# Kernel tuning notes

Measured on AMD Instinct MI355X. Metric: run time of the kernel, lower is better.

## Reference

```python
import jax, jax.numpy as jnp
import numpy as np

N, E, D, C, M = 50000, 600000, 128, 40, 25000


def setup_inputs() -> dict:
    key = jax.random.key(0)
    ks = jax.random.split(key, 10)
    s = 1.0 / np.sqrt(D)
    return {
        "x": jax.random.normal(ks[0], (N, D), jnp.float32),
        "edge_index": jax.random.randint(ks[1], (2, E), 0, N, jnp.int64),
        "node_label_index": jax.random.randint(ks[2], (M,), 0, N, jnp.int64),
        "W0": jax.random.normal(ks[3], (D, D), jnp.float32) * s,
        "b0": jnp.zeros((D,), jnp.float32),
        "W1": jax.random.normal(ks[4], (D, D), jnp.float32) * s,
        "b1": jnp.zeros((D,), jnp.float32),
        "W2": jax.random.normal(ks[5], (D, D), jnp.float32) * s,
        "b2": jnp.zeros((D,), jnp.float32),
        "W3": jax.random.normal(ks[6], (D, D), jnp.float32) * s,
        "b3": jnp.zeros((D,), jnp.float32),
        "Wh": jax.random.normal(ks[7], (D, C), jnp.float32) * s,
        "bh": jnp.zeros((C,), jnp.float32),
    }


def _gcn(x, W, b, src, dst, dinv):
    h = x @ W                                    # [N, D']
    norm = (dinv[src] * dinv[dst])[:, None]      # [E, 1]
    agg = jax.ops.segment_sum(h[src] * norm, dst, num_segments=x.shape[0])
    return agg + h * (dinv ** 2)[:, None] + b    # self-loop term + bias


def reference(x, edge_index, node_label_index, W0, b0, W1, b1, W2, b2, W3, b3, Wh, bh):
    src, dst = edge_index[0], edge_index[1]
    # degree with self-loops (PyG counts in-degree on dst after add_self_loops)
    deg = 1.0 + jax.ops.segment_sum(jnp.ones((src.shape[0],), x.dtype), dst,
                                    num_segments=x.shape[0])
    dinv = jax.lax.rsqrt(deg)

    cell0 = _gcn(x, W0, b0, src, dst, dinv)
    cell1 = _gcn(jax.nn.relu(cell0), W1, b1, src, dst, dinv)
    cell2 = (_gcn(jax.nn.relu(cell0), W2, b2, src, dst, dinv)
             + _gcn(jax.nn.relu(cell1), W2, b2, src, dst, dinv))
    cell3 = (_gcn(jax.nn.relu(cell0), W3, b3, src, dst, dinv)
             + _gcn(jax.nn.relu(cell1), W3, b3, src, dst, dinv)
             + _gcn(jax.nn.relu(cell2), W3, b3, src, dst, dinv))

    feat = jax.nn.log_softmax(cell3, axis=1)
    pred = (feat @ Wh + bh)[node_label_index]    # [M, C]
    return pred
```

## Files before the change

### kernel.cpp

```cpp
#include <hip/hip_runtime.h>
#include <hip/hip_bf16.h>
#include <cstdint>
#include <cstddef>

#define DIM 128

typedef __attribute__((ext_vector_type(8))) short bf16x8;
typedef __attribute__((ext_vector_type(4))) float f32x4;

__device__ __forceinline__ unsigned short f2bf(float f) {
    __hip_bfloat16 h = __float2bfloat16(f);
    return *(unsigned short*)&h;
}
__device__ __forceinline__ unsigned pack_bf2(float a, float b) {
    return (unsigned)f2bf(a) | ((unsigned)f2bf(b) << 16);
}
__device__ __forceinline__ float bflo(unsigned u) { return __uint_as_float(u << 16); }
__device__ __forceinline__ float bfhi(unsigned u) { return __uint_as_float(u & 0xffff0000u); }

union U4B8 { uint4 q; bf16x8 v; };

__global__ __launch_bounds__(256)
void k_init(const int* __restrict__ dst, int* __restrict__ count,
            int* __restrict__ rank, int e, int egrid,
            const float* __restrict__ W0, const float* __restrict__ W1,
            const float* __restrict__ W2, const float* __restrict__ W3,
            const float* __restrict__ Wh, const float* __restrict__ b3,
            const float* __restrict__ bh,
            unsigned short* __restrict__ Wpk,
            unsigned short* __restrict__ WcombP,
            float* __restrict__ whs, float* __restrict__ bcomb,
            unsigned short* __restrict__ H, unsigned short* __restrict__ Abuf,
            float* __restrict__ dinv, int n, int C) {
    if ((int)blockIdx.x < egrid) {
        int i = blockIdx.x * 256 + threadIdx.x;
        if (i < e) rank[i] = atomicAdd(&count[dst[i]], 1);
        return;
    }
    const int NW = 4 * DIM * DIM;
    const int NH = 3 * 4 * 64 * 8;
    int g = (blockIdx.x - egrid) * 256 + threadIdx.x;
    if (g < NW) {
        int j   = g & 7;
        int ln  = (g >> 3) & 63;
        int kc  = (g >> 9) & 3;
        int nt  = (g >> 11) & 7;
        int mat = g >> 14;
        const float* W = (mat == 0) ? W0 : (mat == 1) ? W1 : (mat == 2) ? W2 : W3;
        int k = kc * 32 + (ln >> 4) * 8 + j;
        int nc = nt * 16 + (ln & 15);
        Wpk[g] = f2bf(W[k * DIM + nc]);
    } else if (g < NW + NH) {
        int gg = g - NW;
        int j  = gg & 7;
        int ln = (gg >> 3) & 63;
        int kc = (gg >> 9) & 3;
        int nt = gg >> 11;
        int k  = kc * 32 + (ln >> 4) * 8 + j;
        int nc = nt * 16 + (ln & 15);
        float s = 0.f;
        if (nc < C) {
            for (int d = 0; d < DIM; ++d) s += W3[k * DIM + d] * Wh[d * C + nc];
        }
        WcombP[gg] = f2bf(s);
    } else if (g < NW + NH + 64) {
        int c = g - NW - NH;
        if (c < C) {
            float s = 0.f, t = 0.f;
            for (int d = 0; d < DIM; ++d) {
                float w = Wh[d * C + c];
                s += w;
                t += b3[d] * w;
            }
            whs[c]   = s;
            bcomb[c] = 3.0f * t + bh[c];
        }
    } else if (g < NW + NH + 64 + 16) {
        int t = g - (NW + NH + 64);
        uint4 z; z.x = z.y = z.z = z.w = 0u;
        ((uint4*)H)[(size_t)n * 16 + t] = z;
    } else if (g < NW + NH + 64 + 32) {
        int t = g - (NW + NH + 64 + 16);
        uint4 z; z.x = z.y = z.z = z.w = 0u;
        ((uint4*)Abuf)[(size_t)n * 16 + t] = z;
    } else if (g == NW + NH + 64 + 32) {
        dinv[n] = 0.f;
    }
}

__global__ __launch_bounds__(1024)
void k_scanA(const int* __restrict__ count, int* __restrict__ partial,
             int* __restrict__ bsum, float* __restrict__ dinv, int n) {
    __shared__ int wsum[16];
    int tid = threadIdx.x, lane = tid & 63, wid = tid >> 6;
    int i = blockIdx.x * 1024 + tid;
    int v = (i < n) ? count[i] : 0;
    if (i < n) dinv[i] = rsqrtf(1.0f + (float)v);
    int x = v;
    #pragma unroll
    for (int off = 1; off < 64; off <<= 1) {
        int y = __shfl_up(x, off, 64);
        if (lane >= off) x += y;
    }
    if (lane == 63) wsum[wid] = x;
    __syncthreads();
    int waveoff = 0, total = 0;
    #pragma unroll
    for (int w = 0; w < 16; ++w) {
        int s = wsum[w];
        if (w < wid) waveoff += s;
        total += s;
    }
    if (i < n) partial[i] = x + waveoff;
    if (tid == 0) bsum[blockIdx.x] = total;
}

__global__ __launch_bounds__(1024)
void k_scanB(const int* __restrict__ partial, const int* __restrict__ bsum,
             int* __restrict__ row_ptr, int n, int nb) {
    __shared__ int s_off;
    int tid = threadIdx.x;
    if (tid < 64) {
        int carry = 0;
        for (int base = 0; base < nb; base += 64) {
            int idx = base + tid;
            int v = (idx < nb && idx < blockIdx.x) ? bsum[idx] : 0;
            #pragma unroll
            for (int off = 32; off > 0; off >>= 1) v += __shfl_xor(v, off, 64);
            carry += v;
        }
        if (tid == 0) s_off = carry;
    }
    __syncthreads();
    int off = s_off;
    int i = blockIdx.x * 1024 + tid;
    if (i < n) row_ptr[i + 1] = partial[i] + off;
    if (blockIdx.x == 0 && tid == 0) row_ptr[0] = 0;
}

__global__ __launch_bounds__(256)
void k_fillmm(const float* __restrict__ in, const unsigned short* __restrict__ Wpk,
              const float* __restrict__ dinv, unsigned short* __restrict__ outp, int n,
              const int* __restrict__ src, const int* __restrict__ dst,
              const int* __restrict__ rank, const int* __restrict__ row_ptr,
              int* __restrict__ colv, int e, int mmg) {
    if ((int)blockIdx.x >= mmg) {
        int i = (blockIdx.x - mmg) * 256 + threadIdx.x;
        if (i < e) {
            int d = dst[i];
            int r = rank[i];
            colv[row_ptr[d] + r] = src[i];
        }
        return;
    }
    int wv   = threadIdx.x >> 6;
    int lane = threadIdx.x & 63;
    int r0   = blockIdx.x * 64 + wv * 16;
    int m    = lane & 15;
    int quad = lane >> 4;

    bf16x8 afr[4];
    int arow = r0 + m;
    bool rowok = arow < n;
    const float* ap = in + (size_t)arow * DIM + quad * 8;
    #pragma unroll
    for (int kc = 0; kc < 4; ++kc) {
        float4 p0, p1;
        if (rowok) {
            p0 = *(const float4*)(ap + kc * 32);
            p1 = *(const float4*)(ap + kc * 32 + 4);
        } else {
            p0.x = p0.y = p0.z = p0.w = 0.f;
            p1.x = p1.y = p1.z = p1.w = 0.f;
        }
        union { bf16x8 v; unsigned short u[8]; } a;
        a.u[0] = f2bf(p0.x); a.u[1] = f2bf(p0.y);
        a.u[2] = f2bf(p0.z); a.u[3] = f2bf(p0.w);
        a.u[4] = f2bf(p1.x); a.u[5] = f2bf(p1.y);
        a.u[6] = f2bf(p1.z); a.u[7] = f2bf(p1.w);
        afr[kc] = a.v;
    }

    float dsc[4];
    #pragma unroll
    for (int t = 0; t < 4; ++t) {
        int r = r0 + quad * 4 + t;
        dsc[t] = (r < n) ? dinv[r] : 0.f;
    }

    const uint4* wp = (const uint4*)Wpk;
    #pragma unroll
    for (int nt = 0; nt < 8; ++nt) {
        f32x4 acc = {0.f, 0.f, 0.f, 0.f};
        #pragma unroll
        for (int kc = 0; kc < 4; ++kc) {
            U4B8 b; b.q = wp[(nt * 4 + kc) * 64 + lane];
            acc = __builtin_amdgcn_mfma_f32_16x16x32_bf16(afr[kc], b.v, acc, 0, 0, 0);
        }
        int colb = nt * 16 + m;
        #pragma unroll
        for (int t = 0; t < 4; ++t) {
            int r = r0 + quad * 4 + t;
            if (r < n)
                outp[(size_t)r * DIM + colb] = f2bf(dsc[t] * acc[t]);
        }
    }
}

__global__ __launch_bounds__(256)
void k_matmul_b(const unsigned short* __restrict__ in, const unsigned short* __restrict__ Wpk,
                const float* __restrict__ dinv, unsigned short* __restrict__ outp, int n) {
    int wv   = threadIdx.x >> 6;
    int lane = threadIdx.x & 63;
    int r0   = blockIdx.x * 64 + wv * 16;
    int m    = lane & 15;
    int quad = lane >> 4;

    bf16x8 afr[4];
    int arow = r0 + m;
    bool rowok = arow < n;
    const uint4* in16 = (const uint4*)in;
    #pragma unroll
    for (int kc = 0; kc < 4; ++kc) {
        U4B8 a;
        if (rowok) a.q = in16[(size_t)arow * 16 + kc * 4 + quad];
        else { a.q.x = a.q.y = a.q.z = a.q.w = 0u; }
        afr[kc] = a.v;
    }

    float dsc[4];
    #pragma unroll
    for (int t = 0; t < 4; ++t) {
        int r = r0 + quad * 4 + t;
        dsc[t] = (r < n) ? dinv[r] : 0.f;
    }

    const uint4* wp = (const uint4*)Wpk;
    #pragma unroll
    for (int nt = 0; nt < 8; ++nt) {
        f32x4 acc = {0.f, 0.f, 0.f, 0.f};
        #pragma unroll
        for (int kc = 0; kc < 4; ++kc) {
            U4B8 b; b.q = wp[(nt * 4 + kc) * 64 + lane];
            acc = __builtin_amdgcn_mfma_f32_16x16x32_bf16(afr[kc], b.v, acc, 0, 0, 0);
        }
        int colb = nt * 16 + m;
        #pragma unroll
        for (int t = 0; t < 4; ++t) {
            int r = r0 + quad * 4 + t;
            if (r < n)
                outp[(size_t)r * DIM + colb] = f2bf(dsc[t] * acc[t]);
        }
    }
}

__global__ __launch_bounds__(256)
void k_prop(const unsigned short* __restrict__ h, const int* __restrict__ row_ptr,
            const int* __restrict__ col, const float* __restrict__ dinv,
            const float* __restrict__ bias, float bscale,
            const unsigned short* addin, unsigned short* __restrict__ outp, int n) {
    int node = (blockIdx.x * 256 + threadIdx.x) >> 6;
    int lane = threadIdx.x & 63;
    if (node >= n) return;
    int beg = row_ptr[node], end = row_ptr[node + 1];
    float di = dinv[node];
    int qid = lane >> 4;
    int fo  = lane & 15;
    const uint4* h16 = (const uint4*)h;
    uint4 sd = h16[((unsigned)node << 4) | fo];
    float aL0 = 0.f, aH0 = 0.f, aL1 = 0.f, aH1 = 0.f;
    float aL2 = 0.f, aH2 = 0.f, aL3 = 0.f, aH3 = 0.f;
    float bL0 = 0.f, bH0 = 0.f, bL1 = 0.f, bH1 = 0.f;
    float bL2 = 0.f, bH2 = 0.f, bL3 = 0.f, bH3 = 0.f;
    int j = beg + qid;
    int s0 = (j < end) ? col[j] : n;
    int s1 = (j + 4 < end) ? col[j + 4] : n;
    while (s0 != n) {
        uint4 d0 = h16[((unsigned)s0 << 4) | fo];
        uint4 d1 = h16[((unsigned)s1 << 4) | fo];
        int jn = j + 8;
        s0 = (jn < end) ? col[jn] : n;
        s1 = (jn + 4 < end) ? col[jn + 4] : n;
        j = jn;
        aL0 += bflo(d0.x); aH0 += bfhi(d0.x);
        aL1 += bflo(d0.y); aH1 += bfhi(d0.y);
        aL2 += bflo(d0.z); aH2 += bfhi(d0.z);
        aL3 += bflo(d0.w); aH3 += bfhi(d0.w);
        bL0 += bflo(d1.x); bH0 += bfhi(d1.x);
        bL1 += bflo(d1.y); bH1 += bfhi(d1.y);
        bL2 += bflo(d1.z); bH2 += bfhi(d1.z);
        bL3 += bflo(d1.w); bH3 += bfhi(d1.w);
    }
    uint4 av; av.x = av.y = av.z = av.w = 0u;
    if (addin) av = ((const uint4*)addin)[(size_t)node * 16 + fo];
    aL0 += bL0; aH0 += bH0; aL1 += bL1; aH1 += bH1;
    aL2 += bL2; aH2 += bH2; aL3 += bL3; aH3 += bH3;
    aL0 += __shfl_xor(aL0, 16, 64); aL0 += __shfl_xor(aL0, 32, 64);
    aH0 += __shfl_xor(aH0, 16, 64); aH0 += __shfl_xor(aH0, 32, 64);
    aL1 += __shfl_xor(aL1, 16, 64); aL1 += __shfl_xor(aL1, 32, 64);
    aH1 += __shfl_xor(aH1, 16, 64); aH1 += __shfl_xor(aH1, 32, 64);
    aL2 += __shfl_xor(aL2, 16, 64); aL2 += __shfl_xor(aL2, 32, 64);
    aH2 += __shfl_xor(aH2, 16, 64); aH2 += __shfl_xor(aH2, 32, 64);
    aL3 += __shfl_xor(aL3, 16, 64); aL3 += __shfl_xor(aL3, 32, 64);
    aH3 += __shfl_xor(aH3, 16, 64); aH3 += __shfl_xor(aH3, 32, 64);
    aL0 += bflo(sd.x); aH0 += bfhi(sd.x);
    aL1 += bflo(sd.y); aH1 += bfhi(sd.y);
    aL2 += bflo(sd.z); aH2 += bfhi(sd.z);
    aL3 += bflo(sd.w); aH3 += bfhi(sd.w);
    if (lane < 16) {
        const float4* b4 = (const float4*)bias;
        float4 bA = b4[2 * fo], bB = b4[2 * fo + 1];
        float r0x = fmaxf(fmaf(bscale, bA.x, di * aL0), 0.f);
        float r0y = fmaxf(fmaf(bscale, bA.y, di * aH0), 0.f);
        float r0z = fmaxf(fmaf(bscale, bA.z, di * aL1), 0.f);
        float r0w = fmaxf(fmaf(bscale, bA.w, di * aH1), 0.f);
        float r1x = fmaxf(fmaf(bscale, bB.x, di * aL2), 0.f);
        float r1y = fmaxf(fmaf(bscale, bB.y, di * aH2), 0.f);
        float r1z = fmaxf(fmaf(bscale, bB.z, di * aL3), 0.f);
        float r1w = fmaxf(fmaf(bscale, bB.w, di * aH3), 0.f);
        r0x += bflo(av.x); r0y += bfhi(av.x);
        r0z += bflo(av.y); r0w += bfhi(av.y);
        r1x += bflo(av.z); r1y += bfhi(av.z);
        r1z += bflo(av.w); r1w += bfhi(av.w);
        size_t base = (size_t)node * 16 + fo;
        uint4 o;
        o.x = pack_bf2(r0x, r0y);
        o.y = pack_bf2(r0z, r0w);
        o.z = pack_bf2(r1x, r1y);
        o.w = pack_bf2(r1z, r1w);
        ((uint4*)outp)[base] = o;
    }
}

__global__ __launch_bounds__(1024)
void k_propv_fused(const unsigned short* __restrict__ A, const int* __restrict__ row_ptr,
                   const int* __restrict__ col, const float* __restrict__ dinv,
                   const float* __restrict__ b3, float bscale,
                   const int* __restrict__ labels,
                   const unsigned short* __restrict__ W3pk,
                   const unsigned short* __restrict__ WcombP,
                   const float* __restrict__ whs, const float* __restrict__ bcomb,
                   float* __restrict__ outp, int m_total, int C, int n) {
    __shared__ uint4 Vs[16 * 17];
    __shared__ float Ds[16];
    __shared__ float Mred[8 * 16];
    __shared__ float Sred[8 * 16];
    __shared__ float Ls[16];
    int wid  = threadIdx.x >> 6;
    int lane = threadIdx.x & 63;
    int m = blockIdx.x * 16 + wid;
    bool valid = m < m_total;
    int node = valid ? labels[m] : 0;
    int beg = 0, end = 0;
    if (valid) { beg = row_ptr[node]; end = row_ptr[node + 1]; }
    float di = dinv[node];
    int qid = lane >> 4, fo = lane & 15;
    const uint4* h16 = (const uint4*)A;
    uint4 sd = h16[((unsigned)node << 4) | fo];
    float aL0 = 0.f, aH0 = 0.f, aL1 = 0.f, aH1 = 0.f;
    float aL2 = 0.f, aH2 = 0.f, aL3 = 0.f, aH3 = 0.f;
    float bL0 = 0.f, bH0 = 0.f, bL1 = 0.f, bH1 = 0.f;
    float bL2 = 0.f, bH2 = 0.f, bL3 = 0.f, bH3 = 0.f;
    int j = beg + qid;
    int s0 = (j < end) ? col[j] : n;
    int s1 = (j + 4 < end) ? col[j + 4] : n;
    float w0 = dinv[s0], w1 = dinv[s1];
    while (s0 != n) {
        uint4 d0 = h16[((unsigned)s0 << 4) | fo];
        uint4 d1 = h16[((unsigned)s1 << 4) | fo];
        float cw0 = w0, cw1 = w1;
        int jn = j + 8;
        s0 = (jn < end) ? col[jn] : n;
        s1 = (jn + 4 < end) ? col[jn + 4] : n;
        w0 = dinv[s0]; w1 = dinv[s1];
        j = jn;
        aL0 = fmaf(cw0, bflo(d0.x), aL0); aH0 = fmaf(cw0, bfhi(d0.x), aH0);
        aL1 = fmaf(cw0, bflo(d0.y), aL1); aH1 = fmaf(cw0, bfhi(d0.y), aH1);
        aL2 = fmaf(cw0, bflo(d0.z), aL2); aH2 = fmaf(cw0, bfhi(d0.z), aH2);
        aL3 = fmaf(cw0, bflo(d0.w), aL3); aH3 = fmaf(cw0, bfhi(d0.w), aH3);
        bL0 = fmaf(cw1, bflo(d1.x), bL0); bH0 = fmaf(cw1, bfhi(d1.x), bH0);
        bL1 = fmaf(cw1, bflo(d1.y), bL1); bH1 = fmaf(cw1, bfhi(d1.y), bH1);
        bL2 = fmaf(cw1, bflo(d1.z), bL2); bH2 = fmaf(cw1, bfhi(d1.z), bH2);
        bL3 = fmaf(cw1, bflo(d1.w), bL3); bH3 = fmaf(cw1, bfhi(d1.w), bH3);
    }
    aL0 += bL0; aH0 += bH0; aL1 += bL1; aH1 += bH1;
    aL2 += bL2; aH2 += bH2; aL3 += bL3; aH3 += bH3;
    aL0 += __shfl_xor(aL0, 16, 64); aL0 += __shfl_xor(aL0, 32, 64);
    aH0 += __shfl_xor(aH0, 16, 64); aH0 += __shfl_xor(aH0, 32, 64);
    aL1 += __shfl_xor(aL1, 16, 64); aL1 += __shfl_xor(aL1, 32, 64);
    aH1 += __shfl_xor(aH1, 16, 64); aH1 += __shfl_xor(aH1, 32, 64);
    aL2 += __shfl_xor(aL2, 16, 64); aL2 += __shfl_xor(aL2, 32, 64);
    aH2 += __shfl_xor(aH2, 16, 64); aH2 += __shfl_xor(aH2, 32, 64);
    aL3 += __shfl_xor(aL3, 16, 64); aL3 += __shfl_xor(aL3, 32, 64);
    aH3 += __shfl_xor(aH3, 16, 64); aH3 += __shfl_xor(aH3, 32, 64);
    aL0 = fmaf(di, bflo(sd.x), aL0); aH0 = fmaf(di, bfhi(sd.x), aH0);
    aL1 = fmaf(di, bflo(sd.y), aL1); aH1 = fmaf(di, bfhi(sd.y), aH1);
    aL2 = fmaf(di, bflo(sd.z), aL2); aH2 = fmaf(di, bfhi(sd.z), aH2);
    aL3 = fmaf(di, bflo(sd.w), aL3); aH3 = fmaf(di, bfhi(sd.w), aH3);
    if (lane < 16) {
        uint4 o;
        o.x = pack_bf2(aL0, aH0);
        o.y = pack_bf2(aL1, aH1);
        o.z = pack_bf2(aL2, aH2);
        o.w = pack_bf2(aL3, aH3);
        Vs[wid * 17 + fo] = o;
    }
    if (lane == 0) Ds[wid] = di;
    __syncthreads();

    f32x4 hacc = {0.f, 0.f, 0.f, 0.f};
    float cell[4] = {0.f, 0.f, 0.f, 0.f};
    float gmx[4]  = {0.f, 0.f, 0.f, 0.f};
    int mm = lane & 15, quad = lane >> 4;
    if (wid < 8) {
        int nt = wid;
        bf16x8 afr[4];
        #pragma unroll
        for (int kc = 0; kc < 4; ++kc) {
            U4B8 a; a.q = Vs[mm * 17 + kc * 4 + quad];
            afr[kc] = a.v;
        }
        f32x4 acc = {0.f, 0.f, 0.f, 0.f};
        const uint4* wp = (const uint4*)W3pk;
        #pragma unroll
        for (int kc = 0; kc < 4; ++kc) {
            U4B8 b; b.q = wp[(nt * 4 + kc) * 64 + lane];
            acc = __builtin_amdgcn_mfma_f32_16x16x32_bf16(afr[kc], b.v, acc, 0, 0, 0);
        }
        float b3c = bscale * b3[nt * 16 + mm];
        #pragma unroll
        for (int t = 0; t < 4; ++t) {
            int row = quad * 4 + t;
            cell[t] = fmaf(Ds[row], acc[t], b3c);
            float mxv = cell[t];
            #pragma unroll
            for (int off = 1; off < 16; off <<= 1)
                mxv = fmaxf(mxv, __shfl_xor(mxv, off, 64));
            if (mm == 0) Mred[nt * 16 + row] = mxv;
        }
    } else if (wid < 11) {
        int nth = wid - 8;
        bf16x8 afr[4];
        #pragma unroll
        for (int kc = 0; kc < 4; ++kc) {
            U4B8 a; a.q = Vs[mm * 17 + kc * 4 + quad];
            afr[kc] = a.v;
        }
        const uint4* wp = (const uint4*)WcombP;
        #pragma unroll
        for (int kc = 0; kc < 4; ++kc) {
            U4B8 b; b.q = wp[(nth * 4 + kc) * 64 + lane];
            hacc = __builtin_amdgcn_mfma_f32_16x16x32_bf16(afr[kc], b.v, hacc, 0, 0, 0);
        }
    }
    __syncthreads();

    if (wid < 8) {
        int nt = wid;
        #pragma unroll
        for (int t = 0; t < 4; ++t) {
            int row = quad * 4 + t;
            float g = Mred[row];
            #pragma unroll
            for (int i = 1; i < 8; ++i) g = fmaxf(g, Mred[i * 16 + row]);
            gmx[t] = g;
            float e = expf(cell[t] - g);
            #pragma unroll
            for (int off = 1; off < 16; off <<= 1) e += __shfl_xor(e, off, 64);
            if (mm == 0) Sred[nt * 16 + row] = e;
        }
    }
    __syncthreads();

    if (wid == 0 && mm == 0) {
        #pragma unroll
        for (int t = 0; t < 4; ++t) {
            int row = quad * 4 + t;
            float s = Sred[row];
            #pragma unroll
            for (int i = 1; i < 8; ++i) s += Sred[i * 16 + row];
            Ls[row] = gmx[t] + logf(s);
        }
    }
    __syncthreads();

    if (wid >= 8 && wid < 11) {
        int nth = wid - 8;
        int colc = nth * 16 + mm;
        if (colc < C) {
            float wsc = whs[colc], bc = bcomb[colc];
            #pragma unroll
            for (int t = 0; t < 4; ++t) {
                int row = quad * 4 + t;
                int r = blockIdx.x * 16 + row;
                if (r < m_total)
                    outp[(size_t)r * C + colc] =
                        fmaf(Ds[row], hacc[t], bc) - Ls[row] * wsc;
            }
        }
    }
}

extern "C" void kernel_launch(void* const* d_in, const int* in_sizes, int n_in,
                              void* d_out, int out_size, void* d_ws, size_t ws_size,
                              hipStream_t stream) {
    const float* x      = (const float*)d_in[0];
    const int*   edges  = (const int*)d_in[1];
    const int*   labels = (const int*)d_in[2];
    const float* W0 = (const float*)d_in[3];
    const float* b0 = (const float*)d_in[4];
    const float* W1 = (const float*)d_in[5];
    const float* b1 = (const float*)d_in[6];
    const float* W2 = (const float*)d_in[7];
    const float* b2 = (const float*)d_in[8];
    const float* W3 = (const float*)d_in[9];
    const float* b3 = (const float*)d_in[10];
    const float* Wh = (const float*)d_in[11];
    const float* bh = (const float*)d_in[12];
    float* out = (float*)d_out;

    const int N = in_sizes[0] / DIM;
    const int E = in_sizes[1] / 2;
    const int M = in_sizes[2];
    const int C = in_sizes[12];

    char* ws = (char*)d_ws;
    auto alloc = [&](size_t bytes) {
        char* p = ws;
        ws += (bytes + 255) & ~(size_t)255;
        return p;
    };
    float* dinv    = (float*)alloc((size_t)(N + 1) * 4);
    int*   count   = (int*)  alloc((size_t)N * 4);
    int*   row_ptr = (int*)  alloc((size_t)(N + 1) * 4);
    int*   rank    = (int*)  alloc((size_t)E * 4);
    int*   partial = (int*)  alloc((size_t)N * 4);
    int*   bsum    = (int*)  alloc(64 * 4);
    int*   col     = (int*)  alloc((size_t)E * 4);
    float* whs     = (float*)alloc(256);
    float* bcomb   = (float*)alloc(256);
    unsigned short* Wpk    = (unsigned short*)alloc((size_t)4 * DIM * DIM * 2);
    unsigned short* WcombP = (unsigned short*)alloc((size_t)3 * 4 * 64 * 8 * 2);
    unsigned short* H   = (unsigned short*)alloc((size_t)(N + 1) * DIM * 2);
    unsigned short* R0  = (unsigned short*)alloc((size_t)N * DIM * 2);
    unsigned short* A   = (unsigned short*)alloc((size_t)(N + 1) * DIM * 2);

    const int* src = edges;
    const int* dst = edges + E;

    int egrid  = (E + 255) / 256;
    int sgrid  = (N + 1023) / 1024;
    int mmgrid = (N + 63) / 64;
    int pgrid  = (N + 3) / 4;
    const int FR = DIM * DIM;
    const int NPACK = 4 * FR + 3 * 4 * 64 * 8 + 64 + 33;
    int packgrid = (NPACK + 255) / 256;

    hipMemsetAsync(count, 0, (size_t)N * 4, stream);
    k_init <<<egrid + packgrid, 256, 0, stream>>>(dst, count, rank, E, egrid,
                                                  W0, W1, W2, W3, Wh, b3, bh,
                                                  Wpk, WcombP, whs, bcomb,
                                                  H, A, dinv, N, C);
    k_scanA<<<sgrid, 1024, 0, stream>>>(count, partial, bsum, dinv, N);
    k_scanB<<<sgrid, 1024, 0, stream>>>(partial, bsum, row_ptr, N, sgrid);
    k_fillmm<<<mmgrid + egrid, 256, 0, stream>>>(x, Wpk, dinv, H, N,
                                                 src, dst, rank, row_ptr, col, E, mmgrid);
    k_prop    <<<pgrid, 256, 0, stream>>>(H, row_ptr, col, dinv, b0, 1.f, nullptr, R0, N);
    k_matmul_b<<<mmgrid, 256, 0, stream>>>(R0, Wpk + 1 * FR, dinv, H, N);
    k_prop    <<<pgrid, 256, 0, stream>>>(H, row_ptr, col, dinv, b1, 1.f, R0, A, N);
    k_matmul_b<<<mmgrid, 256, 0, stream>>>(A, Wpk + 2 * FR, dinv, H, N);
    k_prop    <<<pgrid, 256, 0, stream>>>(H, row_ptr, col, dinv, b2, 2.f, A, A, N);
    k_propv_fused<<<(M + 15) / 16, 1024, 0, stream>>>(A, row_ptr, col, dinv, b3, 3.f,
                                                      labels, Wpk + 3 * FR, WcombP,
                                                      whs, bcomb, out, M, C, N);
}
```

Baseline: 282.0 us.

## Fuse sparse propagation with following dense matmul in one kernel

Replaces the prop kernel plus separate matmul kernel pairs with a single kernel that aggregates 16 nodes (one wave per node), stages the relu'd results in shared memory, then has 8 waves compute the next layer's 128x128 MFMA product for those rows. A second H buffer is added so the kernel can read one projection while writing the next. This removes a kernel launch and a global round trip of the activation per layer, at the cost of a block-wide barrier and half the waves idling during the matmul phase.

```diff
diff --git a/kernel.cpp b/kernel.cpp
--- a/kernel.cpp
+++ b/kernel.cpp
@@ -30,7 +30,8 @@
             unsigned short* __restrict__ Wpk,
             unsigned short* __restrict__ WcombP,
             float* __restrict__ whs, float* __restrict__ bcomb,
-            unsigned short* __restrict__ H, unsigned short* __restrict__ Abuf,
+            unsigned short* __restrict__ H, unsigned short* __restrict__ H2,
+            unsigned short* __restrict__ Abuf,
             float* __restrict__ dinv, int n, int C) {
     if ((int)blockIdx.x < egrid) {
         int i = blockIdx.x * 256 + threadIdx.x;
@@ -82,8 +83,12 @@
     } else if (g < NW + NH + 64 + 32) {
         int t = g - (NW + NH + 64 + 16);
         uint4 z; z.x = z.y = z.z = z.w = 0u;
+        ((uint4*)H2)[(size_t)n * 16 + t] = z;
+    } else if (g < NW + NH + 64 + 48) {
+        int t = g - (NW + NH + 64 + 32);
+        uint4 z; z.x = z.y = z.z = z.w = 0u;
         ((uint4*)Abuf)[(size_t)n * 16 + t] = z;
-    } else if (g == NW + NH + 64 + 32) {
+    } else if (g == NW + NH + 64 + 48) {
         dinv[n] = 0.f;
     }
 }
@@ -207,49 +212,115 @@
     }
 }
 
-__global__ __launch_bounds__(256)
-void k_matmul_b(const unsigned short* __restrict__ in, const unsigned short* __restrict__ Wpk,
-                const float* __restrict__ dinv, unsigned short* __restrict__ outp, int n) {
-    int wv   = threadIdx.x >> 6;
+__global__ __launch_bounds__(1024)
+void k_prop_mm(const unsigned short* __restrict__ h, const int* __restrict__ row_ptr,
+               const int* __restrict__ col, const float* __restrict__ dinv,
+               const float* __restrict__ bias, float bscale,
+               const unsigned short* addin, unsigned short* __restrict__ outp,
+               const unsigned short* __restrict__ Wnext,
+               unsigned short* __restrict__ outH, int n) {
+    __shared__ uint4 Vs[16 * 17];
+    __shared__ float Ds[16];
+    int wid  = threadIdx.x >> 6;
     int lane = threadIdx.x & 63;
-    int r0   = blockIdx.x * 64 + wv * 16;
-    int m    = lane & 15;
-    int quad = lane >> 4;
-
-    bf16x8 afr[4];
-    int arow = r0 + m;
-    bool rowok = arow < n;
-    const uint4* in16 = (const uint4*)in;
-    #pragma unroll
-    for (int kc = 0; kc < 4; ++kc) {
-        U4B8 a;
-        if (rowok) a.q = in16[(size_t)arow * 16 + kc * 4 + quad];
-        else { a.q.x = a.q.y = a.q.z = a.q.w = 0u; }
-        afr[kc] = a.v;
-    }
-
-    float dsc[4];
-    #pragma unroll
-    for (int t = 0; t < 4; ++t) {
-        int r = r0 + quad * 4 + t;
-        dsc[t] = (r < n) ? dinv[r] : 0.f;
-    }
-
-    const uint4* wp = (const uint4*)Wpk;
-    #pragma unroll
-    for (int nt = 0; nt < 8; ++nt) {
+    int node = blockIdx.x * 16 + wid;
+    bool valid = node < n;
+    int gnode = valid ? node : 0;
+    int beg = 0, end = 0;
+    if (valid) { beg = row_ptr[gnode]; end = row_ptr[gnode + 1]; }
+    float di = dinv[gnode];
+    int qid = lane >> 4, fo = lane & 15;
+    const uint4* h16 = (const uint4*)h;
+    uint4 sd = h16[((unsigned)gnode << 4) | fo];
+    float aL0 = 0.f, aH0 = 0.f, aL1 = 0.f, aH1 = 0.f;
+    float aL2 = 0.f, aH2 = 0.f, aL3 = 0.f, aH3 = 0.f;
+    float bL0 = 0.f, bH0 = 0.f, bL1 = 0.f, bH1 = 0.f;
+    float bL2 = 0.f, bH2 = 0.f, bL3 = 0.f, bH3 = 0.f;
+    int j = beg + qid;
+    int s0 = (j < end) ? col[j] : n;
+    int s1 = (j + 4 < end) ? col[j + 4] : n;
+    while (s0 != n) {
+        uint4 d0 = h16[((unsigned)s0 << 4) | fo];
+        uint4 d1 = h16[((unsigned)s1 << 4) | fo];
+        int jn = j + 8;
+        s0 = (jn < end) ? col[jn] : n;
+        s1 = (jn + 4 < end) ? col[jn + 4] : n;
+        j = jn;
+        aL0 += bflo(d0.x); aH0 += bfhi(d0.x);
+        aL1 += bflo(d0.y); aH1 += bfhi(d0.y);
+        aL2 += bflo(d0.z); aH2 += bfhi(d0.z);
+        aL3 += bflo(d0.w); aH3 += bfhi(d0.w);
+        bL0 += bflo(d1.x); bH0 += bfhi(d1.x);
+        bL1 += bflo(d1.y); bH1 += bfhi(d1.y);
+        bL2 += bflo(d1.z); bH2 += bfhi(d1.z);
+        bL3 += bflo(d1.w); bH3 += bfhi(d1.w);
+    }
+    uint4 av; av.x = av.y = av.z = av.w = 0u;
+    if (addin) av = ((const uint4*)addin)[(size_t)gnode * 16 + fo];
+    aL0 += bL0; aH0 += bH0; aL1 += bL1; aH1 += bH1;
+    aL2 += bL2; aH2 += bH2; aL3 += bL3; aH3 += bH3;
+    aL0 += __shfl_xor(aL0, 16, 64); aL0 += __shfl_xor(aL0, 32, 64);
+    aH0 += __shfl_xor(aH0, 16, 64); aH0 += __shfl_xor(aH0, 32, 64);
+    aL1 += __shfl_xor(aL1, 16, 64); aL1 += __shfl_xor(aL1, 32, 64);
+    aH1 += __shfl_xor(aH1, 16, 64); aH1 += __shfl_xor(aH1, 32, 64);
+    aL2 += __shfl_xor(aL2, 16, 64); aL2 += __shfl_xor(aL2, 32, 64);
+    aH2 += __shfl_xor(aH2, 16, 64); aH2 += __shfl_xor(aH2, 32, 64);
+    aL3 += __shfl_xor(aL3, 16, 64); aL3 += __shfl_xor(aL3, 32, 64);
+    aH3 += __shfl_xor(aH3, 16, 64); aH3 += __shfl_xor(aH3, 32, 64);
+    aL0 += bflo(sd.x); aH0 += bfhi(sd.x);
+    aL1 += bflo(sd.y); aH1 += bfhi(sd.y);
+    aL2 += bflo(sd.z); aH2 += bfhi(sd.z);
+    aL3 += bflo(sd.w); aH3 += bfhi(sd.w);
+    if (lane < 16) {
+        const float4* b4 = (const float4*)bias;
+        float4 bA = b4[2 * fo], bB = b4[2 * fo + 1];
+        float r0x = fmaxf(fmaf(bscale, bA.x, di * aL0), 0.f);
+        float r0y = fmaxf(fmaf(bscale, bA.y, di * aH0), 0.f);
+        float r0z = fmaxf(fmaf(bscale, bA.z, di * aL1), 0.f);
+        float r0w = fmaxf(fmaf(bscale, bA.w, di * aH1), 0.f);
+        float r1x = fmaxf(fmaf(bscale, bB.x, di * aL2), 0.f);
+        float r1y = fmaxf(fmaf(bscale, bB.y, di * aH2), 0.f);
+        float r1z = fmaxf(fmaf(bscale, bB.z, di * aL3), 0.f);
+        float r1w = fmaxf(fmaf(bscale, bB.w, di * aH3), 0.f);
+        r0x += bflo(av.x); r0y += bfhi(av.x);
+        r0z += bflo(av.y); r0w += bfhi(av.y);
+        r1x += bflo(av.z); r1y += bfhi(av.z);
+        r1z += bflo(av.w); r1w += bfhi(av.w);
+        uint4 o;
+        o.x = pack_bf2(r0x, r0y);
+        o.y = pack_bf2(r0z, r0w);
+        o.z = pack_bf2(r1x, r1y);
+        o.w = pack_bf2(r1z, r1w);
+        Vs[wid * 17 + fo] = o;
+        if (valid)
+            ((uint4*)outp)[(size_t)gnode * 16 + fo] = o;
+        if (fo == 0) Ds[wid] = di;
+    }
+    __syncthreads();
+
+    if (wid < 8) {
+        int nt = wid;
+        int mm = lane & 15, quad = lane >> 4;
+        bf16x8 afr[4];
+        #pragma unroll
+        for (int kc = 0; kc < 4; ++kc) {
+            U4B8 a; a.q = Vs[mm * 17 + kc * 4 + quad];
+            afr[kc] = a.v;
+        }
         f32x4 acc = {0.f, 0.f, 0.f, 0.f};
+        const uint4* wp = (const uint4*)Wnext;
         #pragma unroll
         for (int kc = 0; kc < 4; ++kc) {
             U4B8 b; b.q = wp[(nt * 4 + kc) * 64 + lane];
             acc = __builtin_amdgcn_mfma_f32_16x16x32_bf16(afr[kc], b.v, acc, 0, 0, 0);
         }
-        int colb = nt * 16 + m;
+        int colb = nt * 16 + mm;
         #pragma unroll
         for (int t = 0; t < 4; ++t) {
-            int r = r0 + quad * 4 + t;
+            int row = quad * 4 + t;
+            int r = blockIdx.x * 16 + row;
             if (r < n)
-                outp[(size_t)r * DIM + colb] = f2bf(dsc[t] * acc[t]);
+                outH[(size_t)r * DIM + colb] = f2bf(Ds[row] * acc[t]);
         }
     }
 }
@@ -542,6 +613,7 @@
     unsigned short* Wpk    = (unsigned short*)alloc((size_t)4 * DIM * DIM * 2);
     unsigned short* WcombP = (unsigned short*)alloc((size_t)3 * 4 * 64 * 8 * 2);
     unsigned short* H   = (unsigned short*)alloc((size_t)(N + 1) * DIM * 2);
+    unsigned short* H2  = (unsigned short*)alloc((size_t)(N + 1) * DIM * 2);
     unsigned short* R0  = (unsigned short*)alloc((size_t)N * DIM * 2);
     unsigned short* A   = (unsigned short*)alloc((size_t)(N + 1) * DIM * 2);
 
@@ -552,23 +624,24 @@
     int sgrid  = (N + 1023) / 1024;
     int mmgrid = (N + 63) / 64;
     int pgrid  = (N + 3) / 4;
+    int fgrid  = (N + 15) / 16;
     const int FR = DIM * DIM;
-    const int NPACK = 4 * FR + 3 * 4 * 64 * 8 + 64 + 33;
+    const int NPACK = 4 * FR + 3 * 4 * 64 * 8 + 64 + 49;
     int packgrid = (NPACK + 255) / 256;
 
     hipMemsetAsync(count, 0, (size_t)N * 4, stream);
     k_init <<<egrid + packgrid, 256, 0, stream>>>(dst, count, rank, E, egrid,
                                                   W0, W1, W2, W3, Wh, b3, bh,
                                                   Wpk, WcombP, whs, bcomb,
-                                                  H, A, dinv, N, C);
+                                                  H, H2, A, dinv, N, C);
     k_scanA<<<sgrid, 1024, 0, stream>>>(count, partial, bsum, dinv, N);
     k_scanB<<<sgrid, 1024, 0, stream>>>(partial, bsum, row_ptr, N, sgrid);
     k_fillmm<<<mmgrid + egrid, 256, 0, stream>>>(x, Wpk, dinv, H, N,
                                                  src, dst, rank, row_ptr, col, E, mmgrid);
-    k_prop    <<<pgrid, 256, 0, stream>>>(H, row_ptr, col, dinv, b0, 1.f, nullptr, R0, N);
-    k_matmul_b<<<mmgrid, 256, 0, stream>>>(R0, Wpk + 1 * FR, dinv, H, N);
-    k_prop    <<<pgrid, 256, 0, stream>>>(H, row_ptr, col, dinv, b1, 1.f, R0, A, N);
-    k_matmul_b<<<mmgrid, 256, 0, stream>>>(A, Wpk + 2 * FR, dinv, H, N);
+    k_prop_mm<<<fgrid, 1024, 0, stream>>>(H, row_ptr, col, dinv, b0, 1.f,
+                                          nullptr, R0, Wpk + 1 * FR, H2, N);
+    k_prop_mm<<<fgrid, 1024, 0, stream>>>(H2, row_ptr, col, dinv, b1, 1.f,
+                                          R0, A, Wpk + 2 * FR, H, N);
     k_prop    <<<pgrid, 256, 0, stream>>>(H, row_ptr, col, dinv, b2, 2.f, A, A, N);
     k_propv_fused<<<(M + 15) / 16, 1024, 0, stream>>>(A, row_ptr, col, dinv, b3, 3.f,
                                                       labels, Wpk + 3 * FR, WcombP,
```

Measured after the change: 269.0 us. 1.05x faster.
